# Kernel optimization log

Hardware: AMD Instinct MI355X
Metric: run time of the kernel (lower is better)

## Reference

```python
import jax, jax.numpy as jnp
import numpy as np

N_HOSTS = 16
N_WINDOW = 3
GAT_IN = 3
D = 16          # d_model = gat_output_feats = n_hosts
NHEAD = 2
HD = D // NHEAD # 8
FF = 64
PROTO_DIM = 8
LATENT = N_HOSTS * D * N_WINDOW  # 768
LN_EPS = 1e-5


def _positional_encoding():
    pos = np.arange(N_WINDOW, dtype=np.float32)[:, None]
    div = np.exp(np.arange(0, D, 2, dtype=np.float32) * (-np.log(10000.0) / D))
    pe = np.zeros((N_WINDOW, D), dtype=np.float32)
    pe[:, 0::2] = np.sin(pos * div)
    pe[:, 1::2] = np.cos(pos * div)
    return jnp.asarray(pe[:, None, :])  # (n_window, 1, d_model)


def setup_inputs() -> dict:
    key = jax.random.key(0)
    ks = iter(jax.random.split(key, 40))
    p = lambda *s: jax.random.normal(next(ks), s, dtype=jnp.float32) * 0.05
    inp = {
        't': jax.random.normal(next(ks), (N_WINDOW * N_HOSTS * GAT_IN,), dtype=jnp.float32),
        's': jax.random.normal(next(ks), (N_HOSTS, PROTO_DIM), dtype=jnp.float32),
        # GAT (single head, fully connected 16-node graph)
        'gat_W': p(GAT_IN, D), 'gat_a_src': p(D), 'gat_a_dst': p(D),
        # time encoder Linear(16,16)
        'te_W': p(D, D), 'te_b': p(D),
        'pe': _positional_encoding(),
        # 2 transformer encoder layers, stacked on leading axis
        'qkv_W': p(2, 3 * D, D), 'qkv_b': p(2, 3 * D),
        'out_W': p(2, D, D), 'out_b': p(2, D),
        'ln1_g': jnp.ones((2, D), jnp.float32), 'ln1_b': jnp.zeros((2, D), jnp.float32),
        'ff1_W': p(2, FF, D), 'ff1_b': p(2, FF),
        'ff2_W': p(2, D, FF), 'ff2_b': p(2, D),
        'ln2_g': jnp.ones((2, D), jnp.float32), 'ln2_b': jnp.zeros((2, D), jnp.float32),
        # decoder heads
        'an_W': p(2 * N_HOSTS, LATENT), 'an_b': p(2 * N_HOSTS),
        'pr_W': p(PROTO_DIM * N_HOSTS, LATENT), 'pr_b': p(PROTO_DIM * N_HOSTS),
    }
    return inp


def _layer_norm(x, g, b):
    m = x.mean(-1, keepdims=True)
    v = ((x - m) ** 2).mean(-1, keepdims=True)
    return (x - m) * jax.lax.rsqrt(v + LN_EPS) * g + b


def reference(t, s, gat_W, gat_a_src, gat_a_dst, te_W, te_b, pe,
              qkv_W, qkv_b, out_W, out_b, ln1_g, ln1_b,
              ff1_W, ff1_b, ff2_W, ff2_b, ln2_g, ln2_b,
              an_W, an_b, pr_W, pr_b):
    # --- GAT over fully connected 16-host graph, per window ---
    x = t.reshape(N_WINDOW, N_HOSTS, GAT_IN)
    h = x @ gat_W                                   # (w, n, D)
    e_src = h @ gat_a_src                           # (w, n)
    e_dst = h @ gat_a_dst                           # (w, n)
    e = jax.nn.leaky_relu(e_src[:, :, None] + e_dst[:, None, :], 0.2)  # (w, src, dst)
    alpha = jax.nn.softmax(e, axis=1)               # softmax over sources, per dst
    gat_out = jax.nn.elu(jnp.einsum('wsd,wsf->wdf', alpha, h))         # (w, n, D)
    # --- time encode + positional encode (dropout = identity in eval) ---
    xe = gat_out @ te_W.T + te_b + pe               # (seq=3, batch=16, D)
    # --- 2 post-norm TransformerEncoderLayers ---
    inv_sqrt_hd = 1.0 / np.sqrt(HD).astype(np.float32)
    for l in range(2):
        qkv = xe @ qkv_W[l].T + qkv_b[l]            # (s, b, 3D)
        q, k, v = jnp.split(qkv, 3, axis=-1)
        hd = lambda z: z.reshape(N_WINDOW, N_HOSTS, NHEAD, HD).transpose(1, 2, 0, 3)  # (b,h,s,hd)
        q, k, v = hd(q), hd(k), hd(v)
        att = jax.nn.softmax(jnp.einsum('bhqd,bhkd->bhqk', q, k) * inv_sqrt_hd, axis=-1)
        ctx = jnp.einsum('bhqk,bhkd->bhqd', att, v).transpose(2, 0, 1, 3).reshape(N_WINDOW, N_HOSTS, D)
        xe = _layer_norm(xe + ctx @ out_W[l].T + out_b[l], ln1_g[l], ln1_b[l])
        ff = jax.nn.relu(xe @ ff1_W[l].T + ff1_b[l]) @ ff2_W[l].T + ff2_b[l]
        xe = _layer_norm(xe + ff, ln2_g[l], ln2_b[l])
    # --- flatten to latent (batch-major, matching permute(1,0,2).reshape) ---
    latent = xe.transpose(1, 0, 2).reshape(1, LATENT)
    # nn.LeakyReLU(True): negative_slope=True==1.0, i.e. identity (faithful to source)
    anomaly = jax.nn.leaky_relu(latent @ an_W.T + an_b, 1.0).reshape(N_HOSTS, 2)
    proto = jax.nn.sigmoid(latent @ pr_W.T + pr_b).reshape(N_HOSTS, PROTO_DIM)
    return anomaly, proto
```

## Files before the change

### kernel.cpp

```cpp
#include <hip/hip_runtime.h>
#include <hip/hip_bf16.h>


#define NW 3
#define NHOST 16
#define DM 16
#define FFD 64
#define LAT 768

typedef __hip_bfloat16 bf16;
typedef __attribute__((ext_vector_type(8))) unsigned short ushort8v;
typedef __attribute__((ext_vector_type(4))) unsigned short ushort4v;

static __device__ __forceinline__ float u2f(unsigned short u) {
    return __uint_as_float(((unsigned)u) << 16);
}

static __device__ __forceinline__ float lwf(const unsigned short* smW, int i) { return u2f(smW[i]); }
static __device__ __forceinline__ float lwf(const float* smW, int i) { return smW[i]; }

static __device__ __forceinline__ float gld(const bf16* p, int i) { return __bfloat162float(p[i]); }
static __device__ __forceinline__ float gld(const float* p, int i) { return p[i]; }
static __device__ __forceinline__ void gst(bf16* p, int i, float v) { p[i] = __float2bfloat16(v); }
static __device__ __forceinline__ void gst(float* p, int i, float v) { p[i] = v; }

static __device__ __forceinline__ void ld8g(const bf16* p, float* o) {
    ushort8v v = *(const ushort8v*)p;
    #pragma unroll
    for (int u = 0; u < 8; ++u) o[u] = u2f(v[u]);
}
static __device__ __forceinline__ void ld8g(const float* p, float* o) {
    float4 a = ((const float4*)p)[0], b = ((const float4*)p)[1];
    o[0]=a.x; o[1]=a.y; o[2]=a.z; o[3]=a.w; o[4]=b.x; o[5]=b.y; o[6]=b.z; o[7]=b.w;
}
static __device__ __forceinline__ void ld4g(const bf16* p, float* o) {
    ushort4v v = *(const ushort4v*)p;
    #pragma unroll
    for (int u = 0; u < 4; ++u) o[u] = u2f(v[u]);
}
static __device__ __forceinline__ void ld4g(const float* p, float* o) {
    float4 a = *(const float4*)p;
    o[0]=a.x; o[1]=a.y; o[2]=a.z; o[3]=a.w;
}

enum {
    OFF_T    = 0,
    OFF_GATW = 144,
    OFF_ASRC = 192,
    OFF_ADST = 208,
    OFF_TEW  = 224,
    OFF_TEB  = 480,
    OFF_PE   = 496,
    OFF_QKVW = 544,
    OFF_QKVB = 2080,
    OFF_OUTW = 2176,
    OFF_OUTB = 2688,
    OFF_LN1G = 2720,
    OFF_LN1B = 2752,
    OFF_FF1W = 2784,
    OFF_FF1B = 4832,
    OFF_FF2W = 4960,
    OFF_FF2B = 7008,
    OFF_LN2G = 7040,
    OFF_LN2B = 7072,
    TOTAL_W  = 7104
};

struct Smem {
    float h[NW][NHOST][DM];
    float esrc[NW][NHOST];
    float edst[NW][NHOST];
    float alpha[NW][NHOST][NHOST];
    float xe[NW][NHOST][DM];
    float qkv[NW][NHOST][48];
    float ctx[NW][NHOST][DM];
    float tmp[NW][NHOST][DM];
    float ffh[NW][NHOST][FFD];
};

template<typename T, typename WT>
__device__ void encode_impl(Smem& sm, WT* smW, int tid,
    const T* tin, const T* gatW, const T* asrc, const T* adst,
    const T* teW, const T* teb, const T* pe_,
    const T* qkvW, const T* qkvb, const T* outW, const T* outb,
    const T* ln1g, const T* ln1b,
    const T* ff1W, const T* ff1b, const T* ff2W, const T* ff2b,
    const T* ln2g, const T* ln2b,
    float* latent_out)
{
    constexpr int EPC = 16 / (int)sizeof(T);
    constexpr int NCHUNK = TOTAL_W / EPC;
    for (int g = tid; g < NCHUNK; g += 256) {
        int e = g * EPC;
        const T* p; int base;
        if      (e < OFF_GATW) { p = tin;   base = OFF_T; }
        else if (e < OFF_ASRC) { p = gatW;  base = OFF_GATW; }
        else if (e < OFF_ADST) { p = asrc;  base = OFF_ASRC; }
        else if (e < OFF_TEW)  { p = adst;  base = OFF_ADST; }
        else if (e < OFF_TEB)  { p = teW;   base = OFF_TEW; }
        else if (e < OFF_PE)   { p = teb;   base = OFF_TEB; }
        else if (e < OFF_QKVW) { p = pe_;   base = OFF_PE; }
        else if (e < OFF_QKVB) { p = qkvW;  base = OFF_QKVW; }
        else if (e < OFF_OUTW) { p = qkvb;  base = OFF_QKVB; }
        else if (e < OFF_OUTB) { p = outW;  base = OFF_OUTW; }
        else if (e < OFF_LN1G) { p = outb;  base = OFF_OUTB; }
        else if (e < OFF_LN1B) { p = ln1g;  base = OFF_LN1G; }
        else if (e < OFF_FF1W) { p = ln1b;  base = OFF_LN1B; }
        else if (e < OFF_FF1B) { p = ff1W;  base = OFF_FF1W; }
        else if (e < OFF_FF2W) { p = ff1b;  base = OFF_FF1B; }
        else if (e < OFF_FF2B) { p = ff2W;  base = OFF_FF2W; }
        else if (e < OFF_LN2G) { p = ff2b;  base = OFF_FF2B; }
        else if (e < OFF_LN2B) { p = ln2g;  base = OFF_LN2G; }
        else                   { p = ln2b;  base = OFF_LN2B; }
        *(ushort8v*)((unsigned char*)smW + (size_t)e * sizeof(T)) =
            *(const ushort8v*)(p + (e - base));
    }
    __syncthreads();

    for (int idx = tid; idx < NW * NHOST * DM; idx += 256) {
        int w = idx >> 8, r = idx & 255, n = r >> 4, f = r & 15;
        float acc = 0.f;
        #pragma unroll
        for (int i = 0; i < 3; ++i)
            acc += lwf(smW, OFF_T + (w * NHOST + n) * 3 + i) * lwf(smW, OFF_GATW + i * DM + f);
        sm.h[w][n][f] = acc;
    }
    __syncthreads();

    if (tid < 96) {
        int w = tid / 32, r = tid % 32, n = r & 15, which = r >> 4;
        int abase = which ? OFF_ADST : OFF_ASRC;
        float acc = 0.f;
        #pragma unroll
        for (int f = 0; f < DM; ++f) acc += sm.h[w][n][f] * lwf(smW, abase + f);
        if (which) sm.edst[w][n] = acc; else sm.esrc[w][n] = acc;
    }
    __syncthreads();

    if (tid < 48) {
        int w = tid / 16, d = tid & 15;
        float ed = sm.edst[w][d];
        float e[16];
        float mx = -1e30f;
        #pragma unroll
        for (int s = 0; s < 16; ++s) {
            float x = sm.esrc[w][s] + ed;
            x = x > 0.f ? x : 0.2f * x;
            e[s] = x;
            mx = fmaxf(mx, x);
        }
        float sum = 0.f;
        #pragma unroll
        for (int s = 0; s < 16; ++s) { e[s] = __expf(e[s] - mx); sum += e[s]; }
        float inv = 1.f / sum;
        #pragma unroll
        for (int s = 0; s < 16; ++s) sm.alpha[w][s][d] = e[s] * inv;
    }
    __syncthreads();

    for (int idx = tid; idx < NW * NHOST * DM; idx += 256) {
        int w = idx >> 8, r = idx & 255, d = r >> 4, f = r & 15;
        float acc = 0.f;
        #pragma unroll
        for (int s = 0; s < 16; ++s) acc += sm.alpha[w][s][d] * sm.h[w][s][f];
        sm.tmp[w][d][f] = acc > 0.f ? acc : (__expf(acc) - 1.f);
    }
    __syncthreads();

    for (int idx = tid; idx < NW * NHOST * DM; idx += 256) {
        int w = idx >> 8, r = idx & 255, n = r >> 4, f = r & 15;
        float acc = lwf(smW, OFF_TEB + f) + lwf(smW, OFF_PE + w * DM + f);
        #pragma unroll
        for (int g = 0; g < DM; ++g)
            acc += sm.tmp[w][n][g] * lwf(smW, OFF_TEW + f * DM + g);
        sm.xe[w][n][f] = acc;
    }
    __syncthreads();

    for (int l = 0; l < 2; ++l) {
        int qW = OFF_QKVW + l * 768, qb = OFF_QKVB + l * 48;
        for (int idx = tid; idx < NW * NHOST * 48; idx += 256) {
            int w = idx / (NHOST * 48), r = idx % (NHOST * 48), n = r / 48, j = r % 48;
            float acc = lwf(smW, qb + j);
            #pragma unroll
            for (int f = 0; f < DM; ++f) acc += sm.xe[w][n][f] * lwf(smW, qW + j * DM + f);
            sm.qkv[w][n][j] = acc;
        }
        __syncthreads();

        if (tid < 96) {
            int b = tid / 6, r = tid % 6, hh = r / 3, qs = r % 3;
            const float inv_sqrt_hd = 0.35355339059327373f;
            float sc[3];
            #pragma unroll
            for (int ks = 0; ks < 3; ++ks) {
                float acc = 0.f;
                #pragma unroll
                for (int d0 = 0; d0 < 8; ++d0)
                    acc += sm.qkv[qs][b][hh * 8 + d0] * sm.qkv[ks][b][16 + hh * 8 + d0];
                sc[ks] = acc * inv_sqrt_hd;
            }
            float mx = fmaxf(sc[0], fmaxf(sc[1], sc[2]));
            float s0 = __expf(sc[0] - mx), s1 = __expf(sc[1] - mx), s2 = __expf(sc[2] - mx);
            float inv = 1.f / (s0 + s1 + s2);
            s0 *= inv; s1 *= inv; s2 *= inv;
            #pragma unroll
            for (int d0 = 0; d0 < 8; ++d0)
                sm.ctx[qs][b][hh * 8 + d0] = s0 * sm.qkv[0][b][32 + hh * 8 + d0]
                                           + s1 * sm.qkv[1][b][32 + hh * 8 + d0]
                                           + s2 * sm.qkv[2][b][32 + hh * 8 + d0];
        }
        __syncthreads();

        int oW = OFF_OUTW + l * 256, ob = OFF_OUTB + l * 16;
        for (int idx = tid; idx < NW * NHOST * DM; idx += 256) {
            int w = idx >> 8, r = idx & 255, n = r >> 4, f = r & 15;
            float acc = lwf(smW, ob + f) + sm.xe[w][n][f];
            #pragma unroll
            for (int g = 0; g < DM; ++g) acc += sm.ctx[w][n][g] * lwf(smW, oW + f * DM + g);
            sm.tmp[w][n][f] = acc;
        }
        __syncthreads();

        if (tid < 48) {
            int w = tid / 16, n = tid & 15;
            float m = 0.f;
            #pragma unroll
            for (int f = 0; f < DM; ++f) m += sm.tmp[w][n][f];
            m *= (1.f / 16.f);
            float v = 0.f;
            #pragma unroll
            for (int f = 0; f < DM; ++f) { float d0 = sm.tmp[w][n][f] - m; v += d0 * d0; }
            v *= (1.f / 16.f);
            float rr = rsqrtf(v + 1e-5f);
            #pragma unroll
            for (int f = 0; f < DM; ++f)
                sm.xe[w][n][f] = (sm.tmp[w][n][f] - m) * rr * lwf(smW, OFF_LN1G + l * DM + f)
                               + lwf(smW, OFF_LN1B + l * DM + f);
        }
        __syncthreads();

        int f1W = OFF_FF1W + l * 1024, f1b = OFF_FF1B + l * 64;
        for (int idx = tid; idx < NW * NHOST * FFD; idx += 256) {
            int w = idx / (NHOST * FFD), r = idx % (NHOST * FFD), n = r / FFD, j = r % FFD;
            float acc = lwf(smW, f1b + j);
            #pragma unroll
            for (int f = 0; f < DM; ++f) acc += sm.xe[w][n][f] * lwf(smW, f1W + j * DM + f);
            sm.ffh[w][n][j] = fmaxf(acc, 0.f);
        }
        __syncthreads();

        int f2W = OFF_FF2W + l * 1024, f2b = OFF_FF2B + l * 16;
        for (int idx = tid; idx < NW * NHOST * DM; idx += 256) {
            int w = idx >> 8, r = idx & 255, n = r >> 4, f = r & 15;
            float acc = lwf(smW, f2b + f) + sm.xe[w][n][f];
            #pragma unroll
            for (int j = 0; j < FFD; ++j) acc += sm.ffh[w][n][j] * lwf(smW, f2W + f * FFD + j);
            sm.tmp[w][n][f] = acc;
        }
        __syncthreads();

        if (tid < 48) {
            int w = tid / 16, n = tid & 15;
            float m = 0.f;
            #pragma unroll
            for (int f = 0; f < DM; ++f) m += sm.tmp[w][n][f];
            m *= (1.f / 16.f);
            float v = 0.f;
            #pragma unroll
            for (int f = 0; f < DM; ++f) { float d0 = sm.tmp[w][n][f] - m; v += d0 * d0; }
            v *= (1.f / 16.f);
            float rr = rsqrtf(v + 1e-5f);
            #pragma unroll
            for (int f = 0; f < DM; ++f)
                sm.xe[w][n][f] = (sm.tmp[w][n][f] - m) * rr * lwf(smW, OFF_LN2G + l * DM + f)
                               + lwf(smW, OFF_LN2B + l * DM + f);
        }
        __syncthreads();
    }

    for (int idx = tid; idx < LAT; idx += 256) {
        int w = idx >> 8, r = idx & 255, n = r >> 4, f = r & 15;
        latent_out[n * 48 + w * DM + f] = sm.xe[w][n][f];
    }
}

__global__ void __launch_bounds__(256) txf_encode(
    const void* t, const void* gat_W, const void* a_src, const void* a_dst,
    const void* te_W, const void* te_b, const void* pe,
    const void* qkv_W, const void* qkv_b, const void* out_W, const void* out_b,
    const void* ln1_g, const void* ln1_b,
    const void* ff1_W, const void* ff1_b, const void* ff2_W, const void* ff2_b,
    const void* ln2_g, const void* ln2_b,
    float* latent_out)
{
    __shared__ Smem sm;
    __shared__ __align__(16) unsigned char wbuf[TOTAL_W * 4];
    const int tid = threadIdx.x;
    unsigned w0 = *(const unsigned*)ln1_g;
    if (w0 == 0x3F803F80u) {
        encode_impl<bf16, unsigned short>(sm, (unsigned short*)wbuf, tid,
            (const bf16*)t, (const bf16*)gat_W, (const bf16*)a_src, (const bf16*)a_dst,
            (const bf16*)te_W, (const bf16*)te_b, (const bf16*)pe,
            (const bf16*)qkv_W, (const bf16*)qkv_b, (const bf16*)out_W, (const bf16*)out_b,
            (const bf16*)ln1_g, (const bf16*)ln1_b,
            (const bf16*)ff1_W, (const bf16*)ff1_b, (const bf16*)ff2_W, (const bf16*)ff2_b,
            (const bf16*)ln2_g, (const bf16*)ln2_b, latent_out);
    } else {
        encode_impl<float, float>(sm, (float*)wbuf, tid,
            (const float*)t, (const float*)gat_W, (const float*)a_src, (const float*)a_dst,
            (const float*)te_W, (const float*)te_b, (const float*)pe,
            (const float*)qkv_W, (const float*)qkv_b, (const float*)out_W, (const float*)out_b,
            (const float*)ln1_g, (const float*)ln1_b,
            (const float*)ff1_W, (const float*)ff1_b, (const float*)ff2_W, (const float*)ff2_b,
            (const float*)ln2_g, (const float*)ln2_b, latent_out);
    }
}

template<typename T>
__device__ void decode_impl(const T* an_W, const T* an_b, const T* pr_W, const T* pr_b,
                            const float* latent, T* out)
{
    const int o = blockIdx.x;
    const int l = threadIdx.x;
    const T* Wr = (o < 32) ? (an_W + o * LAT) : (pr_W + (o - 32) * LAT);

    float wv8[8], wv4[4];
    ld8g(Wr + l * 8, wv8);
    ld4g(Wr + 512 + l * 4, wv4);
    float4 a = ((const float4*)latent)[2 * l];
    float4 b = ((const float4*)latent)[2 * l + 1];
    float4 c = ((const float4*)(latent + 512))[l];

    float acc = wv8[0]*a.x + wv8[1]*a.y + wv8[2]*a.z + wv8[3]*a.w
              + wv8[4]*b.x + wv8[5]*b.y + wv8[6]*b.z + wv8[7]*b.w
              + wv4[0]*c.x + wv4[1]*c.y + wv4[2]*c.z + wv4[3]*c.w;

    #pragma unroll
    for (int m = 1; m < 64; m <<= 1) acc += __shfl_xor(acc, m);

    if (l == 0) {
        if (o < 32) {
            gst(out, o, acc + gld(an_b, o));
        } else {
            float z = acc + gld(pr_b, o - 32);
            gst(out, o, 1.f / (1.f + __expf(-z)));
        }
    }
}

__global__ void __launch_bounds__(64) txf_decode(
    const void* an_W, const void* an_b, const void* pr_W, const void* pr_b,
    const void* ln1_g, const float* latent, void* out)
{
    unsigned w0 = *(const unsigned*)ln1_g;
    if (w0 == 0x3F803F80u) {
        decode_impl<bf16>((const bf16*)an_W, (const bf16*)an_b,
                          (const bf16*)pr_W, (const bf16*)pr_b, latent, (bf16*)out);
    } else {
        decode_impl<float>((const float*)an_W, (const float*)an_b,
                           (const float*)pr_W, (const float*)pr_b, latent, (float*)out);
    }
}

extern "C" void kernel_launch(void* const* d_in, const int* in_sizes, int n_in,
                              void* d_out, int out_size, void* d_ws, size_t ws_size,
                              hipStream_t stream) {
    float* latent = (float*)d_ws;

    txf_encode<<<1, 256, 0, stream>>>(
        d_in[0],
        d_in[2], d_in[3], d_in[4],
        d_in[5], d_in[6], d_in[7],
        d_in[8], d_in[9], d_in[10], d_in[11],
        d_in[12], d_in[13],
        d_in[14], d_in[15], d_in[16], d_in[17],
        d_in[18], d_in[19],
        latent);

    txf_decode<<<160, 64, 0, stream>>>(
        d_in[20], d_in[21], d_in[22], d_in[23],
        d_in[12],
        latent, d_out);
}
```

Before: 122.6 us.

## Run transformer encoder in a single wavefront with per-token registers and shuffles

```diff
diff --git a/kernel.cpp b/kernel.cpp
--- a/kernel.cpp
+++ b/kernel.cpp
@@ -16,9 +16,6 @@
     return __uint_as_float(((unsigned)u) << 16);
 }
 
-static __device__ __forceinline__ float lwf(const unsigned short* smW, int i) { return u2f(smW[i]); }
-static __device__ __forceinline__ float lwf(const float* smW, int i) { return smW[i]; }
-
 static __device__ __forceinline__ float gld(const bf16* p, int i) { return __bfloat162float(p[i]); }
 static __device__ __forceinline__ float gld(const float* p, int i) { return p[i]; }
 static __device__ __forceinline__ void gst(bf16* p, int i, float v) { p[i] = __float2bfloat16(v); }
@@ -44,42 +41,29 @@
 }
 
 enum {
-    OFF_T    = 0,
-    OFF_GATW = 144,
-    OFF_ASRC = 192,
-    OFF_ADST = 208,
-    OFF_TEW  = 224,
-    OFF_TEB  = 480,
-    OFF_PE   = 496,
-    OFF_QKVW = 544,
-    OFF_QKVB = 2080,
-    OFF_OUTW = 2176,
-    OFF_OUTB = 2688,
-    OFF_LN1G = 2720,
-    OFF_LN1B = 2752,
-    OFF_FF1W = 2784,
-    OFF_FF1B = 4832,
-    OFF_FF2W = 4960,
-    OFF_FF2B = 7008,
-    OFF_LN2G = 7040,
-    OFF_LN2B = 7072,
-    TOTAL_W  = 7104
+    OFF_GATW = 0,
+    OFF_ASRC = 48,
+    OFF_ADST = 64,
+    OFF_TEW  = 80,
+    OFF_TEB  = 336,
+    OFF_PE   = 352,
+    OFF_QKVW = 400,
+    OFF_QKVB = 1936,
+    OFF_OUTW = 2032,
+    OFF_OUTB = 2544,
+    OFF_LN1G = 2576,
+    OFF_LN1B = 2608,
+    OFF_FF1W = 2640,
+    OFF_FF1B = 4688,
+    OFF_FF2W = 4816,
+    OFF_FF2B = 6864,
+    OFF_LN2G = 6896,
+    OFF_LN2B = 6928,
+    TOTAL_W  = 6960
 };
 
-struct Smem {
-    float h[NW][NHOST][DM];
-    float esrc[NW][NHOST];
-    float edst[NW][NHOST];
-    float alpha[NW][NHOST][NHOST];
-    float xe[NW][NHOST][DM];
-    float qkv[NW][NHOST][48];
-    float ctx[NW][NHOST][DM];
-    float tmp[NW][NHOST][DM];
-    float ffh[NW][NHOST][FFD];
-};
-
-template<typename T, typename WT>
-__device__ void encode_impl(Smem& sm, WT* smW, int tid,
+template<typename T>
+__device__ void encode_impl(float* smW, float* hsh, int tid,
     const T* tin, const T* gatW, const T* asrc, const T* adst,
     const T* teW, const T* teb, const T* pe_,
     const T* qkvW, const T* qkvb, const T* outW, const T* outb,
@@ -88,13 +72,11 @@
     const T* ln2g, const T* ln2b,
     float* latent_out)
 {
-    constexpr int EPC = 16 / (int)sizeof(T);
-    constexpr int NCHUNK = TOTAL_W / EPC;
+    constexpr int NCHUNK = TOTAL_W / 8;
     for (int g = tid; g < NCHUNK; g += 256) {
-        int e = g * EPC;
+        int e = g * 8;
         const T* p; int base;
-        if      (e < OFF_GATW) { p = tin;   base = OFF_T; }
-        else if (e < OFF_ASRC) { p = gatW;  base = OFF_GATW; }
+        if      (e < OFF_ASRC) { p = gatW;  base = OFF_GATW; }
         else if (e < OFF_ADST) { p = asrc;  base = OFF_ASRC; }
         else if (e < OFF_TEW)  { p = adst;  base = OFF_ADST; }
         else if (e < OFF_TEB)  { p = teW;   base = OFF_TEW; }
@@ -112,176 +94,196 @@
         else if (e < OFF_LN2G) { p = ff2b;  base = OFF_FF2B; }
         else if (e < OFF_LN2B) { p = ln2g;  base = OFF_LN2G; }
         else                   { p = ln2b;  base = OFF_LN2B; }
-        *(ushort8v*)((unsigned char*)smW + (size_t)e * sizeof(T)) =
-            *(const ushort8v*)(p + (e - base));
+        float v[8];
+        ld8g(p + (e - base), v);
+        if (e >= OFF_FF2W && e < OFF_FF2B) {
+            #pragma unroll
+            for (int u = 0; u < 8; ++u) {
+                int se = e - OFF_FF2W + u;
+                int l = se >> 10, r = se & 1023, f = r >> 6, j = r & 63;
+                smW[OFF_FF2W + (l << 10) + j * 16 + f] = v[u];
+            }
+        } else {
+            *(float4*)&smW[e]     = float4{v[0], v[1], v[2], v[3]};
+            *(float4*)&smW[e + 4] = float4{v[4], v[5], v[6], v[7]};
+        }
     }
     __syncthreads();
-
-    for (int idx = tid; idx < NW * NHOST * DM; idx += 256) {
-        int w = idx >> 8, r = idx & 255, n = r >> 4, f = r & 15;
+    if (tid >= 64) return;
+
+    const int lane = tid;
+    const int tok  = lane < 48 ? lane : 47;
+    const int w = tok >> 4, n = tok & 15;
+
+    float t0 = gld(tin, tok * 3 + 0), t1 = gld(tin, tok * 3 + 1), t2 = gld(tin, tok * 3 + 2);
+    float h[16];
+    #pragma unroll
+    for (int f = 0; f < 16; ++f) {
         float acc = 0.f;
-        #pragma unroll
-        for (int i = 0; i < 3; ++i)
-            acc += lwf(smW, OFF_T + (w * NHOST + n) * 3 + i) * lwf(smW, OFF_GATW + i * DM + f);
-        sm.h[w][n][f] = acc;
-    }
-    __syncthreads();
-
-    if (tid < 96) {
-        int w = tid / 32, r = tid % 32, n = r & 15, which = r >> 4;
-        int abase = which ? OFF_ADST : OFF_ASRC;
-        float acc = 0.f;
-        #pragma unroll
-        for (int f = 0; f < DM; ++f) acc += sm.h[w][n][f] * lwf(smW, abase + f);
-        if (which) sm.edst[w][n] = acc; else sm.esrc[w][n] = acc;
-    }
-    __syncthreads();
-
-    if (tid < 48) {
-        int w = tid / 16, d = tid & 15;
-        float ed = sm.edst[w][d];
-        float e[16];
-        float mx = -1e30f;
-        #pragma unroll
-        for (int s = 0; s < 16; ++s) {
-            float x = sm.esrc[w][s] + ed;
-            x = x > 0.f ? x : 0.2f * x;
-            e[s] = x;
-            mx = fmaxf(mx, x);
-        }
-        float sum = 0.f;
-        #pragma unroll
-        for (int s = 0; s < 16; ++s) { e[s] = __expf(e[s] - mx); sum += e[s]; }
-        float inv = 1.f / sum;
-        #pragma unroll
-        for (int s = 0; s < 16; ++s) sm.alpha[w][s][d] = e[s] * inv;
-    }
-    __syncthreads();
-
-    for (int idx = tid; idx < NW * NHOST * DM; idx += 256) {
-        int w = idx >> 8, r = idx & 255, d = r >> 4, f = r & 15;
-        float acc = 0.f;
-        #pragma unroll
-        for (int s = 0; s < 16; ++s) acc += sm.alpha[w][s][d] * sm.h[w][s][f];
-        sm.tmp[w][d][f] = acc > 0.f ? acc : (__expf(acc) - 1.f);
-    }
-    __syncthreads();
-
-    for (int idx = tid; idx < NW * NHOST * DM; idx += 256) {
-        int w = idx >> 8, r = idx & 255, n = r >> 4, f = r & 15;
-        float acc = lwf(smW, OFF_TEB + f) + lwf(smW, OFF_PE + w * DM + f);
-        #pragma unroll
-        for (int g = 0; g < DM; ++g)
-            acc += sm.tmp[w][n][g] * lwf(smW, OFF_TEW + f * DM + g);
-        sm.xe[w][n][f] = acc;
-    }
-    __syncthreads();
+        acc += t0 * smW[OFF_GATW + f];
+        acc += t1 * smW[OFF_GATW + 16 + f];
+        acc += t2 * smW[OFF_GATW + 32 + f];
+        h[f] = acc;
+    }
+    float es = 0.f, ed = 0.f;
+    #pragma unroll
+    for (int f = 0; f < 16; ++f) es += h[f] * smW[OFF_ASRC + f];
+    #pragma unroll
+    for (int f = 0; f < 16; ++f) ed += h[f] * smW[OFF_ADST + f];
+
+    if (lane < 48) {
+        #pragma unroll
+        for (int q = 0; q < 4; ++q)
+            *(float4*)&hsh[tok * 16 + q * 4] =
+                float4{h[q*4], h[q*4+1], h[q*4+2], h[q*4+3]};
+    }
+    asm volatile("s_waitcnt lgkmcnt(0)" ::: "memory");
+    __builtin_amdgcn_wave_barrier();
+
+    float e[16];
+    float mx = -1e30f;
+    #pragma unroll
+    for (int s = 0; s < 16; ++s) {
+        float xv = __shfl(es, (tok & 48) + s) + ed;
+        xv = xv > 0.f ? xv : 0.2f * xv;
+        e[s] = xv;
+        mx = fmaxf(mx, xv);
+    }
+    float sum = 0.f;
+    #pragma unroll
+    for (int s = 0; s < 16; ++s) { e[s] = __expf(e[s] - mx); sum += e[s]; }
+    float inv = 1.f / sum;
+
+    float go[16];
+    #pragma unroll
+    for (int f = 0; f < 16; ++f) go[f] = 0.f;
+    #pragma unroll
+    for (int s = 0; s < 16; ++s) {
+        float as = e[s] * inv;
+        const float* hp = &hsh[(((w << 4) + s) << 4)];
+        #pragma unroll
+        for (int f = 0; f < 16; ++f) go[f] += as * hp[f];
+    }
+    #pragma unroll
+    for (int f = 0; f < 16; ++f) go[f] = go[f] > 0.f ? go[f] : __expf(go[f]) - 1.f;
+
+    float x[16];
+    #pragma unroll
+    for (int f = 0; f < 16; ++f) {
+        float acc = smW[OFF_TEB + f] + smW[OFF_PE + (w << 4) + f];
+        #pragma unroll
+        for (int g2 = 0; g2 < 16; ++g2) acc += go[g2] * smW[OFF_TEW + (f << 4) + g2];
+        x[f] = acc;
+    }
 
     for (int l = 0; l < 2; ++l) {
-        int qW = OFF_QKVW + l * 768, qb = OFF_QKVB + l * 48;
-        for (int idx = tid; idx < NW * NHOST * 48; idx += 256) {
-            int w = idx / (NHOST * 48), r = idx % (NHOST * 48), n = r / 48, j = r % 48;
-            float acc = lwf(smW, qb + j);
-            #pragma unroll
-            for (int f = 0; f < DM; ++f) acc += sm.xe[w][n][f] * lwf(smW, qW + j * DM + f);
-            sm.qkv[w][n][j] = acc;
-        }
-        __syncthreads();
-
-        if (tid < 96) {
-            int b = tid / 6, r = tid % 6, hh = r / 3, qs = r % 3;
-            const float inv_sqrt_hd = 0.35355339059327373f;
-            float sc[3];
-            #pragma unroll
-            for (int ks = 0; ks < 3; ++ks) {
+        const int qW = OFF_QKVW + l * 768, qb = OFF_QKVB + l * 48;
+        float qk[48];
+        #pragma unroll
+        for (int j = 0; j < 48; ++j) {
+            float acc = smW[qb + j];
+            #pragma unroll
+            for (int f = 0; f < 16; ++f) acc += x[f] * smW[qW + j * 16 + f];
+            qk[j] = acc;
+        }
+
+        const float inv_sqrt_hd = 0.35355339059327373f;
+        float sc[2][3];
+        #pragma unroll
+        for (int ks = 0; ks < 3; ++ks) {
+            int src = (tok & 15) + (ks << 4);
+            float kk[16];
+            #pragma unroll
+            for (int d = 0; d < 16; ++d) kk[d] = __shfl(qk[16 + d], src);
+            #pragma unroll
+            for (int h2 = 0; h2 < 2; ++h2) {
                 float acc = 0.f;
                 #pragma unroll
-                for (int d0 = 0; d0 < 8; ++d0)
-                    acc += sm.qkv[qs][b][hh * 8 + d0] * sm.qkv[ks][b][16 + hh * 8 + d0];
-                sc[ks] = acc * inv_sqrt_hd;
+                for (int d = 0; d < 8; ++d) acc += qk[h2 * 8 + d] * kk[h2 * 8 + d];
+                sc[h2][ks] = acc * inv_sqrt_hd;
             }
-            float mx = fmaxf(sc[0], fmaxf(sc[1], sc[2]));
-            float s0 = __expf(sc[0] - mx), s1 = __expf(sc[1] - mx), s2 = __expf(sc[2] - mx);
-            float inv = 1.f / (s0 + s1 + s2);
-            s0 *= inv; s1 *= inv; s2 *= inv;
-            #pragma unroll
-            for (int d0 = 0; d0 < 8; ++d0)
-                sm.ctx[qs][b][hh * 8 + d0] = s0 * sm.qkv[0][b][32 + hh * 8 + d0]
-                                           + s1 * sm.qkv[1][b][32 + hh * 8 + d0]
-                                           + s2 * sm.qkv[2][b][32 + hh * 8 + d0];
-        }
-        __syncthreads();
-
-        int oW = OFF_OUTW + l * 256, ob = OFF_OUTB + l * 16;
-        for (int idx = tid; idx < NW * NHOST * DM; idx += 256) {
-            int w = idx >> 8, r = idx & 255, n = r >> 4, f = r & 15;
-            float acc = lwf(smW, ob + f) + sm.xe[w][n][f];
-            #pragma unroll
-            for (int g = 0; g < DM; ++g) acc += sm.ctx[w][n][g] * lwf(smW, oW + f * DM + g);
-            sm.tmp[w][n][f] = acc;
-        }
-        __syncthreads();
-
-        if (tid < 48) {
-            int w = tid / 16, n = tid & 15;
+        }
+        float a[2][3];
+        #pragma unroll
+        for (int h2 = 0; h2 < 2; ++h2) {
+            float m2 = fmaxf(sc[h2][0], fmaxf(sc[h2][1], sc[h2][2]));
+            float s0 = __expf(sc[h2][0] - m2), s1 = __expf(sc[h2][1] - m2), s2 = __expf(sc[h2][2] - m2);
+            float iv = 1.f / (s0 + s1 + s2);
+            a[h2][0] = s0 * iv; a[h2][1] = s1 * iv; a[h2][2] = s2 * iv;
+        }
+        float ctx[16];
+        #pragma unroll
+        for (int ks = 0; ks < 3; ++ks) {
+            int src = (tok & 15) + (ks << 4);
+            #pragma unroll
+            for (int d = 0; d < 16; ++d) {
+                float vv = __shfl(qk[32 + d], src);
+                float av = a[d >> 3][ks];
+                ctx[d] = (ks == 0) ? av * vv : ctx[d] + av * vv;
+            }
+        }
+
+        const int oW = OFF_OUTW + l * 256, ob = OFF_OUTB + l * 16;
+        float r[16];
+        #pragma unroll
+        for (int f = 0; f < 16; ++f) {
+            float acc = smW[ob + f] + x[f];
+            #pragma unroll
+            for (int g2 = 0; g2 < 16; ++g2) acc += ctx[g2] * smW[oW + f * 16 + g2];
+            r[f] = acc;
+        }
+
+        {
             float m = 0.f;
             #pragma unroll
-            for (int f = 0; f < DM; ++f) m += sm.tmp[w][n][f];
+            for (int f = 0; f < 16; ++f) m += r[f];
             m *= (1.f / 16.f);
             float v = 0.f;
             #pragma unroll
-            for (int f = 0; f < DM; ++f) { float d0 = sm.tmp[w][n][f] - m; v += d0 * d0; }
+            for (int f = 0; f < 16; ++f) { float d0 = r[f] - m; v += d0 * d0; }
             v *= (1.f / 16.f);
             float rr = rsqrtf(v + 1e-5f);
             #pragma unroll
-            for (int f = 0; f < DM; ++f)
-                sm.xe[w][n][f] = (sm.tmp[w][n][f] - m) * rr * lwf(smW, OFF_LN1G + l * DM + f)
-                               + lwf(smW, OFF_LN1B + l * DM + f);
-        }
-        __syncthreads();
-
-        int f1W = OFF_FF1W + l * 1024, f1b = OFF_FF1B + l * 64;
-        for (int idx = tid; idx < NW * NHOST * FFD; idx += 256) {
-            int w = idx / (NHOST * FFD), r = idx % (NHOST * FFD), n = r / FFD, j = r % FFD;
-            float acc = lwf(smW, f1b + j);
-            #pragma unroll
-            for (int f = 0; f < DM; ++f) acc += sm.xe[w][n][f] * lwf(smW, f1W + j * DM + f);
-            sm.ffh[w][n][j] = fmaxf(acc, 0.f);
-        }
-        __syncthreads();
-
-        int f2W = OFF_FF2W + l * 1024, f2b = OFF_FF2B + l * 16;
-        for (int idx = tid; idx < NW * NHOST * DM; idx += 256) {
-            int w = idx >> 8, r = idx & 255, n = r >> 4, f = r & 15;
-            float acc = lwf(smW, f2b + f) + sm.xe[w][n][f];
-            #pragma unroll
-            for (int j = 0; j < FFD; ++j) acc += sm.ffh[w][n][j] * lwf(smW, f2W + f * FFD + j);
-            sm.tmp[w][n][f] = acc;
-        }
-        __syncthreads();
-
-        if (tid < 48) {
-            int w = tid / 16, n = tid & 15;
+            for (int f = 0; f < 16; ++f)
+                x[f] = (r[f] - m) * rr * smW[OFF_LN1G + l * 16 + f] + smW[OFF_LN1B + l * 16 + f];
+        }
+
+        const int f1W = OFF_FF1W + l * 1024, f1b = OFF_FF1B + l * 64;
+        const int f2W = OFF_FF2W + l * 1024, f2b = OFF_FF2B + l * 16;
+        float fa[16];
+        #pragma unroll
+        for (int f = 0; f < 16; ++f) fa[f] = smW[f2b + f] + x[f];
+        #pragma unroll 8
+        for (int j = 0; j < 64; ++j) {
+            float hj = smW[f1b + j];
+            #pragma unroll
+            for (int f = 0; f < 16; ++f) hj += x[f] * smW[f1W + j * 16 + f];
+            hj = fmaxf(hj, 0.f);
+            #pragma unroll
+            for (int f = 0; f < 16; ++f) fa[f] += hj * smW[f2W + j * 16 + f];
+        }
+
+        {
             float m = 0.f;
             #pragma unroll
-            for (int f = 0; f < DM; ++f) m += sm.tmp[w][n][f];
+            for (int f = 0; f < 16; ++f) m += fa[f];
             m *= (1.f / 16.f);
             float v = 0.f;
             #pragma unroll
-            for (int f = 0; f < DM; ++f) { float d0 = sm.tmp[w][n][f] - m; v += d0 * d0; }
+            for (int f = 0; f < 16; ++f) { float d0 = fa[f] - m; v += d0 * d0; }
             v *= (1.f / 16.f);
             float rr = rsqrtf(v + 1e-5f);
             #pragma unroll
-            for (int f = 0; f < DM; ++f)
-                sm.xe[w][n][f] = (sm.tmp[w][n][f] - m) * rr * lwf(smW, OFF_LN2G + l * DM + f)
-                               + lwf(smW, OFF_LN2B + l * DM + f);
-        }
-        __syncthreads();
-    }
-
-    for (int idx = tid; idx < LAT; idx += 256) {
-        int w = idx >> 8, r = idx & 255, n = r >> 4, f = r & 15;
-        latent_out[n * 48 + w * DM + f] = sm.xe[w][n][f];
+            for (int f = 0; f < 16; ++f)
+                x[f] = (fa[f] - m) * rr * smW[OFF_LN2G + l * 16 + f] + smW[OFF_LN2B + l * 16 + f];
+        }
+    }
+
+    if (lane < 48) {
+        float* lp = latent_out + n * 48 + w * 16;
+        #pragma unroll
+        for (int q = 0; q < 4; ++q)
+            *(float4*)&lp[q * 4] = float4{x[q*4], x[q*4+1], x[q*4+2], x[q*4+3]};
     }
 }
 
@@ -294,12 +296,12 @@
     const void* ln2_g, const void* ln2_b,
     float* latent_out)
 {
-    __shared__ Smem sm;
-    __shared__ __align__(16) unsigned char wbuf[TOTAL_W * 4];
+    __shared__ float smW[TOTAL_W];
+    __shared__ float hsh[NW * NHOST * DM];
     const int tid = threadIdx.x;
     unsigned w0 = *(const unsigned*)ln1_g;
     if (w0 == 0x3F803F80u) {
-        encode_impl<bf16, unsigned short>(sm, (unsigned short*)wbuf, tid,
+        encode_impl<bf16>(smW, hsh, tid,
             (const bf16*)t, (const bf16*)gat_W, (const bf16*)a_src, (const bf16*)a_dst,
             (const bf16*)te_W, (const bf16*)te_b, (const bf16*)pe,
             (const bf16*)qkv_W, (const bf16*)qkv_b, (const bf16*)out_W, (const bf16*)out_b,
@@ -307,7 +309,7 @@
             (const bf16*)ff1_W, (const bf16*)ff1_b, (const bf16*)ff2_W, (const bf16*)ff2_b,
             (const bf16*)ln2_g, (const bf16*)ln2_b, latent_out);
     } else {
-        encode_impl<float, float>(sm, (float*)wbuf, tid,
+        encode_impl<float>(smW, hsh, tid,
             (const float*)t, (const float*)gat_W, (const float*)a_src, (const float*)a_dst,
             (const float*)te_W, (const float*)te_b, (const float*)pe,
             (const float*)qkv_W, (const float*)qkv_b, (const float*)out_W, (const float*)out_b,
```

Result: slower. 153.5 us (+25.2%).
